# Kernel optimization log

Hardware: AMD Instinct MI355X
Metric: run time of the kernel (lower is better)

## Reference

```python
import jax, jax.numpy as jnp
import numpy as np

B, S, IN_DIM, D, H, L = 2, 2048, 64, 512, 8, 2
DK = D // H
EPS = 1e-5

def _layernorm(x, g, b):
    mu = jnp.mean(x, axis=-1, keepdims=True)
    var = jnp.mean((x - mu) ** 2, axis=-1, keepdims=True)
    return (x - mu) * jax.lax.rsqrt(var + EPS) * g + b

def _prob_sparse_layer(x, Wq, bq, Wk, bk, Wv, bv, fcW, fcb, ln_g, ln_b):
    # x: [B, S, D]
    Bs, Ss, _ = x.shape
    Q = (x @ Wq + bq).reshape(Bs, Ss, H, DK).transpose(0, 2, 1, 3)  # [B,H,S,DK]
    K = (x @ Wk + bk).reshape(Bs, Ss, H, DK).transpose(0, 2, 1, 3)
    V = (x @ Wv + bv).reshape(Bs, Ss, H, DK).transpose(0, 2, 1, 3)
    scores = jnp.einsum('bhqd,bhkd->bhqk', Q, K) / np.sqrt(DK).astype(np.float32)
    k = max(1, Ss // 10)
    top_scores, _ = jax.lax.top_k(scores, k)          # [B,H,S,k]
    threshold = top_scores[..., -1:]                  # k-th largest per row
    sparse_scores = jnp.where(scores < threshold, -jnp.inf, scores)
    attn = jax.nn.softmax(sparse_scores, axis=-1)     # dropout is identity in eval
    out = jnp.einsum('bhqk,bhkd->bhqd', attn, V)
    out = out.transpose(0, 2, 1, 3).reshape(Bs, Ss, D)
    out = out @ fcW + fcb
    return _layernorm(x + out, ln_g, ln_b)

def setup_inputs() -> dict:
    key = jax.random.key(0)
    ks = jax.random.split(key, 16)
    sd = 1.0 / np.sqrt(D)
    sdi = 1.0 / np.sqrt(IN_DIM)
    return {
        'x': jax.random.normal(ks[0], (B, S, IN_DIM), jnp.float32),
        'enc_W': jax.random.normal(ks[1], (IN_DIM, D), jnp.float32) * sdi,
        'enc_b': jnp.zeros((D,), jnp.float32),
        'Wq': jax.random.normal(ks[2], (L, D, D), jnp.float32) * sd,
        'bq': jnp.zeros((L, D), jnp.float32),
        'Wk': jax.random.normal(ks[3], (L, D, D), jnp.float32) * sd,
        'bk': jnp.zeros((L, D), jnp.float32),
        'Wv': jax.random.normal(ks[4], (L, D, D), jnp.float32) * sd,
        'bv': jnp.zeros((L, D), jnp.float32),
        'fcW': jax.random.normal(ks[5], (L, D, D), jnp.float32) * sd,
        'fcb': jnp.zeros((L, D), jnp.float32),
        'ln_g': jnp.ones((L, D), jnp.float32),
        'ln_b': jnp.zeros((L, D), jnp.float32),
        'dec_W': jax.random.normal(ks[6], (D, IN_DIM), jnp.float32) * sd,
        'dec_b': jnp.zeros((IN_DIM,), jnp.float32),
    }

def reference(x, enc_W, enc_b, Wq, bq, Wk, bk, Wv, bv, fcW, fcb, ln_g, ln_b, dec_W, dec_b):
    h = x @ enc_W + enc_b  # [B,S,D]
    for i in range(Wq.shape[0]):
        h = _prob_sparse_layer(h, Wq[i], bq[i], Wk[i], bk[i], Wv[i], bv[i],
                               fcW[i], fcb[i], ln_g[i], ln_b[i])
    return h[:, -1, :] @ dec_W + dec_b  # [B, IN_DIM]
```

## Files before the change

### kernel.cpp

```cpp
#include <hip/hip_runtime.h>
#include <hip/hip_bf16.h>

typedef unsigned short u16;
typedef __bf16 bf16x8 __attribute__((ext_vector_type(8)));
typedef u16 u16x8 __attribute__((ext_vector_type(8)));
typedef float f32x4 __attribute__((ext_vector_type(4)));

#define S_LEN 2048
#define NH 8
#define DMODEL 512
#define TOPK 204

__device__ __forceinline__ u16 f2b(float f) {
  __hip_bfloat16 h = __float2bfloat16(f);
  return __builtin_bit_cast(u16, h);
}
__device__ __forceinline__ unsigned f2b_fast(float f) {
  unsigned u = __float_as_uint(f);
  return (u + 0x7FFFu + ((u >> 16) & 1u)) >> 16;
}
__device__ __forceinline__ float kunmap(unsigned k) {
  unsigned tb = (k & 0x8000u) ? (k ^ 0x8000u) : (~k & 0xFFFFu);
  return __uint_as_float(tb << 16);
}
__device__ __forceinline__ unsigned fkmap(float f) {
  unsigned b = __float_as_uint(f) >> 16;
  return b ^ ((b & 0x8000u) ? 0xFFFFu : 0x8000u);
}

__global__ void transpose_w(const float* __restrict__ in, u16* __restrict__ out, int R, int C) {
  __shared__ float tile[32][33];
  int c0 = blockIdx.x * 32, r0 = blockIdx.y * 32;
  int tx = threadIdx.x & 31, ty = threadIdx.x >> 5;
#pragma unroll
  for (int i = 0; i < 32; i += 8)
    tile[ty + i][tx] = in[(long long)(r0 + ty + i) * C + c0 + tx];
  __syncthreads();
#pragma unroll
  for (int i = 0; i < 32; i += 8)
    out[(long long)(c0 + ty + i) * R + r0 + tx] = f2b(tile[tx][ty + i]);
}

__global__ void transpose_w4(const float* __restrict__ W0, const float* __restrict__ W1,
                             const float* __restrict__ W2, const float* __restrict__ W3,
                             u16* __restrict__ O0, u16* __restrict__ O1,
                             u16* __restrict__ O2, u16* __restrict__ O3) {
  __shared__ float tile[32][33];
  const float* in;
  u16* out;
  switch (blockIdx.z) {
    case 0: in = W0; out = O0; break;
    case 1: in = W1; out = O1; break;
    case 2: in = W2; out = O2; break;
    default: in = W3; out = O3; break;
  }
  int c0 = blockIdx.x * 32, r0 = blockIdx.y * 32;
  int tx = threadIdx.x & 31, ty = threadIdx.x >> 5;
#pragma unroll
  for (int i = 0; i < 32; i += 8)
    tile[ty + i][tx] = in[(long long)(r0 + ty + i) * 512 + c0 + tx];
  __syncthreads();
#pragma unroll
  for (int i = 0; i < 32; i += 8)
    out[(long long)(c0 + ty + i) * 512 + r0 + tx] = f2b(tile[tx][ty + i]);
}

__global__ void conv_b(const float* __restrict__ in, u16* __restrict__ out, int n) {
  int i = blockIdx.x * 256 + threadIdx.x;
  if (i < n) out[i] = f2b(in[i]);
}

template <int MODE>
__global__ __launch_bounds__(256) void gemm_bt(
    const u16* __restrict__ A, const u16* __restrict__ BT,
    const float* __restrict__ bias, const float* __restrict__ biasK, const float* __restrict__ biasV,
    float* __restrict__ outF, u16* __restrict__ outB, u16* __restrict__ outBK, u16* __restrict__ outBV,
    int M, int N, int K, float scale) {
  __shared__ u16 As[64 * 32];
  __shared__ u16 Bs[128 * 32];
  int n0 = blockIdx.x * 128, m0 = blockIdx.y * 64;
  int t = threadIdx.x;
  int lane = t & 63, wv = t >> 6;
  int mw = (wv & 1) * 32, nw = (wv >> 1) * 64;
  int fr = lane & 15, fg = lane >> 4;
  f32x4 acc[2][4] = {};
  for (int kt = 0; kt < K; kt += 32) {
    int e0 = t * 8;
    int r0r = e0 >> 5, c0c = e0 & 31;
    int e1 = e0 + 2048;
    int r1r = e1 >> 5, c1c = e1 & 31;
    *(u16x8*)&As[e0] = *(const u16x8*)&A[(long long)(m0 + r0r) * K + kt + c0c];
    *(u16x8*)&Bs[e0] = *(const u16x8*)&BT[(long long)(n0 + r0r) * K + kt + c0c];
    *(u16x8*)&Bs[e1] = *(const u16x8*)&BT[(long long)(n0 + r1r) * K + kt + c1c];
    __syncthreads();
    bf16x8 af[2], bfv[4];
#pragma unroll
    for (int i = 0; i < 2; i++) af[i] = *(const bf16x8*)&As[(mw + i * 16 + fr) * 32 + fg * 8];
#pragma unroll
    for (int j = 0; j < 4; j++) bfv[j] = *(const bf16x8*)&Bs[(nw + j * 16 + fr) * 32 + fg * 8];
#pragma unroll
    for (int i = 0; i < 2; i++)
#pragma unroll
      for (int j = 0; j < 4; j++)
        acc[i][j] = __builtin_amdgcn_mfma_f32_16x16x32_bf16(af[i], bfv[j], acc[i][j], 0, 0, 0);
    __syncthreads();
  }
#pragma unroll
  for (int i = 0; i < 2; i++)
#pragma unroll
    for (int j = 0; j < 4; j++) {
      int mloc = mw + i * 16 + fg * 4;
      int n = n0 + nw + j * 16 + fr;
      float bvl;
      if constexpr (MODE == 5) {
        int seg = n >> 9, nn = n & 511;
        bvl = (seg == 0 ? bias : seg == 1 ? biasK : biasV)[nn];
      } else {
        bvl = bias ? bias[n] : 0.f;
      }
#pragma unroll
      for (int r = 0; r < 4; r++) {
        int m = m0 + mloc + r;
        float v = acc[i][j][r] * scale + bvl;
        if constexpr (MODE == 0) {
          outF[(long long)m * N + n] = v;
        } else if constexpr (MODE == 4) {
          outF[(long long)m * N + n] = v;
          outB[(long long)m * N + n] = f2b(v);
        } else if constexpr (MODE == 5) {
          int seg = n >> 9, nn = n & 511;
          if (seg == 0) v *= 0.125f;
          u16 val = f2b(v);
          if (seg == 2) {
            outBV[((long long)((m >> 11) * NH + (nn >> 6)) * 64 + (nn & 63)) * S_LEN + (m & 2047)] = val;
          } else {
            long long qkidx = (long long)((m >> 11) * NH + (nn >> 6)) * (S_LEN * 64) +
                              (long long)(m & 2047) * 64 + (nn & 63);
            if (seg == 0) outB[qkidx] = val;
            else outBK[qkidx] = val;
          }
        }
      }
    }
}

__global__ __launch_bounds__(1024, 8) void score_pv(
    const u16* __restrict__ Qb, const u16* __restrict__ Kb, const u16* __restrict__ VTb,
    u16* __restrict__ aoB) {
  __shared__ u16 Qs[16 * 64];
  __shared__ __align__(16) u16 Ss[16 * 2048];
  __shared__ float thrS[16];
  __shared__ float mS[16];
  __shared__ float zS[16 * 16];
  int flat = blockIdx.x;
  int xcd = flat & 7, local = flat >> 3;
  int bh = xcd * 2 + (local >> 7);
  int m0 = (local & 127) * 16;
  int t = threadIdx.x;
  int lane = t & 63, wv = t >> 6, fr = lane & 15, fg = lane >> 4;
  const u16* Qg = Qb + ((long long)bh * S_LEN + m0) * 64;
  const u16* Kg = Kb + (long long)bh * S_LEN * 64;
  const u16* Vg = VTb + (long long)bh * 64 * S_LEN;
  if (t < 128) {
    int row = t >> 3, cc = t & 7;
    *(u16x8*)&Qs[row * 64 + ((cc ^ (row & 7)) * 8)] = *(const u16x8*)&Qg[row * 64 + cc * 8];
  }
  __syncthreads();
  bf16x8 aq[2];
#pragma unroll
  for (int ks = 0; ks < 2; ks++)
    aq[ks] = *(const bf16x8*)&Qs[fr * 64 + (((fg + 4 * ks) ^ (fr & 7)) * 8)];

#pragma unroll 4
  for (int tt = 0; tt < 8; tt++) {
    int col0 = wv * 128 + tt * 16;
    f32x4 acc = {};
#pragma unroll
    for (int ks = 0; ks < 2; ks++) {
      bf16x8 bk = *(const bf16x8*)&Kg[(long long)(col0 + fr) * 64 + ks * 32 + fg * 8];
      acc = __builtin_amdgcn_mfma_f32_16x16x32_bf16(bk, aq[ks], acc, 0, 0, 0);
    }
    uint2 w;
    w.x = f2b_fast(acc[0]) | (f2b_fast(acc[1]) << 16);
    w.y = f2b_fast(acc[2]) | (f2b_fast(acc[3]) << 16);
    int row = fr, col = col0 + fg * 4;
    *(uint2*)&Ss[row * 2048 + (col ^ ((row & 15) << 3))] = w;
  }
  __syncthreads();

  {
    int rr = wv;
    const uint2* cu2 = (const uint2*)&Ss[rr * 2048];
    float kf[32];
#pragma unroll
    for (int j = 0; j < 8; j++) {
      uint2 w = cu2[lane + 64 * j];
      kf[4 * j + 0] = __uint_as_float(w.x << 16);
      kf[4 * j + 1] = __uint_as_float(w.x & 0xFFFF0000u);
      kf[4 * j + 2] = __uint_as_float(w.y << 16);
      kf[4 * j + 3] = __uint_as_float(w.y & 0xFFFF0000u);
    }
    float mxf = kf[0];
#pragma unroll
    for (int j = 1; j < 32; j++) mxf = fmaxf(mxf, kf[j]);
#pragma unroll
    for (int o = 1; o < 64; o <<= 1)
      mxf = fmaxf(mxf, __uint_as_float((unsigned)__shfl_xor((int)__float_as_uint(mxf), o)));
    unsigned mxi = fkmap(mxf);
    unsigned lo, hi;
    unsigned lo0 = mxi > 384u ? mxi - 384u : 0u;
    {
      float pf = kunmap(lo0);
      int c = 0;
#pragma unroll
      for (int j = 0; j < 32; j++) c += (int)__popcll(__ballot(kf[j] >= pf));
      if (c >= TOPK) { lo = lo0; hi = mxi; }
      else { lo = 0u; hi = lo0 - 1u; }
    }
    while (lo < hi) {
      unsigned mid = (lo + hi + 1u) >> 1;
      float midf = kunmap(mid);
      int c = 0;
#pragma unroll
      for (int j = 0; j < 32; j++) c += (int)__popcll(__ballot(kf[j] >= midf));
      if (c >= TOPK) lo = mid; else hi = mid - 1u;
    }
    if (lane == 0) {
      thrS[rr] = kunmap(lo);
      mS[rr] = mxf;
    }
  }
  __syncthreads();

  float thrF = thrS[fr];
  float myM = mS[fr];
  float zpart = 0.f;
  f32x4 acc_o[4] = {};
#pragma unroll 2
  for (int step = 0; step < 4; step++) {
    int k0 = wv * 128 + step * 32;
    u16x8 kk = *(const u16x8*)&Ss[fr * 2048 + ((k0 + fg * 8) ^ ((fr & 15) << 3))];
    unsigned wp[4];
#pragma unroll
    for (int e2 = 0; e2 < 4; e2++) {
      float s0 = __uint_as_float((unsigned)kk[2 * e2] << 16);
      float s1 = __uint_as_float((unsigned)kk[2 * e2 + 1] << 16);
      float p0 = (s0 >= thrF) ? __expf(s0 - myM) : 0.f;
      float p1 = (s1 >= thrF) ? __expf(s1 - myM) : 0.f;
      zpart += p0 + p1;
      wp[e2] = f2b_fast(p0) | (f2b_fast(p1) << 16);
    }
    bf16x8 pa = *(bf16x8*)&wp;
#pragma unroll
    for (int j = 0; j < 4; j++) {
      bf16x8 bv = *(const bf16x8*)&Vg[(long long)(j * 16 + fr) * 2048 + k0 + fg * 8];
      acc_o[j] = __builtin_amdgcn_mfma_f32_16x16x32_bf16(pa, bv, acc_o[j], 0, 0, 0);
    }
  }
  zpart += __shfl_xor(zpart, 16);
  zpart += __shfl_xor(zpart, 32);
  __syncthreads();

  float* Of = (float*)Ss;
#pragma unroll
  for (int j = 0; j < 4; j++)
#pragma unroll
    for (int r = 0; r < 4; r++) {
      int row = fg * 4 + r, col = j * 16 + fr;
      Of[wv * 1024 + row * 64 + (col ^ ((row >> 2) << 3))] = acc_o[j][r];
    }
  if (fg == 0) zS[wv * 16 + fr] = zpart;
  __syncthreads();
  long long ob = (long long)(bh >> 3) * S_LEN * DMODEL + (bh & 7) * 64;
  {
    int row = t >> 6, dk = t & 63;
    int sw = dk ^ ((row >> 2) << 3);
    float s = 0.f;
#pragma unroll
    for (int w = 0; w < 16; w++) s += Of[w * 1024 + row * 64 + sw];
    float z = 0.f;
#pragma unroll
    for (int w = 0; w < 16; w++) z += zS[w * 16 + row];
    aoB[ob + (long long)(m0 + row) * DMODEL + dk] = f2b(s / z);
  }
}

__global__ __launch_bounds__(256) void resid_ln(const float* __restrict__ h, const float* __restrict__ fco,
                                                const float* __restrict__ g, const float* __restrict__ b,
                                                float* __restrict__ hout, u16* __restrict__ hbout) {
  __shared__ float red[4];
  int row = blockIdx.x;
  int t = threadIdx.x;
  long long base = (long long)row * 512;
  float v0 = h[base + t] + fco[base + t];
  float v1 = h[base + t + 256] + fco[base + t + 256];
  float s = v0 + v1;
#pragma unroll
  for (int o = 32; o > 0; o >>= 1) s += __shfl_down(s, o);
  if ((t & 63) == 0) red[t >> 6] = s;
  __syncthreads();
  float mu = (red[0] + red[1] + red[2] + red[3]) * (1.f / 512.f);
  float d0 = v0 - mu, d1 = v1 - mu;
  float q = d0 * d0 + d1 * d1;
#pragma unroll
  for (int o = 32; o > 0; o >>= 1) q += __shfl_down(q, o);
  __syncthreads();
  if ((t & 63) == 0) red[t >> 6] = q;
  __syncthreads();
  float var = (red[0] + red[1] + red[2] + red[3]) * (1.f / 512.f);
  float rs = rsqrtf(var + 1e-5f);
  float y0 = d0 * rs * g[t] + b[t];
  float y1 = d1 * rs * g[t + 256] + b[t + 256];
  hout[base + t] = y0;
  hout[base + t + 256] = y1;
  hbout[base + t] = f2b(y0);
  hbout[base + t + 256] = f2b(y1);
}

__global__ void decoder_k(const float* __restrict__ h, const float* __restrict__ W,
                          const float* __restrict__ bias, float* __restrict__ out) {
  int t = threadIdx.x;
  int b = t >> 6, j = t & 63;
  const float* hr = h + ((long long)b * S_LEN + (S_LEN - 1)) * DMODEL;
  float s = 0.f;
  for (int d = 0; d < DMODEL; d++) s += hr[d] * W[(long long)d * 64 + j];
  out[t] = s + bias[j];
}

extern "C" void kernel_launch(void* const* d_in, const int* in_sizes, int n_in,
                              void* d_out, int out_size, void* d_ws, size_t ws_size,
                              hipStream_t stream) {
  const float* x = (const float*)d_in[0];
  const float* enc_W = (const float*)d_in[1];
  const float* enc_b = (const float*)d_in[2];
  const float* Wq = (const float*)d_in[3];
  const float* bq = (const float*)d_in[4];
  const float* Wk = (const float*)d_in[5];
  const float* bk = (const float*)d_in[6];
  const float* Wv = (const float*)d_in[7];
  const float* bv = (const float*)d_in[8];
  const float* fcW = (const float*)d_in[9];
  const float* fcb = (const float*)d_in[10];
  const float* ln_g = (const float*)d_in[11];
  const float* ln_b = (const float*)d_in[12];
  const float* dec_W = (const float*)d_in[13];
  const float* dec_b = (const float*)d_in[14];

  char* p = (char*)d_ws;
  auto alloc = [&](size_t bytes) {
    char* r = p;
    p += (bytes + 255) & ~(size_t)255;
    return r;
  };
  const size_t BS = 2 * (size_t)S_LEN;
  u16* encWT = (u16*)alloc(512 * 64 * 2);
  u16* xbf = (u16*)alloc(BS * 64 * 2);
  float* hF = (float*)alloc(BS * 512 * 4);
  u16* hB = (u16*)alloc(BS * 512 * 2);
  u16* WqT = (u16*)alloc(512 * 512 * 2);
  u16* WkT = (u16*)alloc(512 * 512 * 2);
  u16* WvT = (u16*)alloc(512 * 512 * 2);
  u16* fcWT = (u16*)alloc(512 * 512 * 2);
  u16* Qb = (u16*)alloc((size_t)16 * 2048 * 64 * 2);
  u16* Kb = (u16*)alloc((size_t)16 * 2048 * 64 * 2);
  u16* VTb = (u16*)alloc((size_t)16 * 2048 * 64 * 2);
  u16* aoB = (u16*)alloc(BS * 512 * 2);
  float* fcO = (float*)Qb;

  transpose_w<<<dim3(16, 2), 256, 0, stream>>>(enc_W, encWT, 64, 512);
  conv_b<<<(int)(BS * 64 / 256), 256, 0, stream>>>(x, xbf, (int)(BS * 64));
  gemm_bt<4><<<dim3(4, 64), 256, 0, stream>>>(xbf, encWT, enc_b, nullptr, nullptr,
                                              hF, hB, nullptr, nullptr, 4096, 512, 64, 1.f);

  for (int l = 0; l < 2; l++) {
    transpose_w4<<<dim3(16, 16, 4), 256, 0, stream>>>(
        Wq + (size_t)l * 512 * 512, Wk + (size_t)l * 512 * 512,
        Wv + (size_t)l * 512 * 512, fcW + (size_t)l * 512 * 512,
        WqT, WkT, WvT, fcWT);
    gemm_bt<5><<<dim3(12, 64), 256, 0, stream>>>(hB, WqT, bq + l * 512, bk + l * 512, bv + l * 512,
                                                 nullptr, Qb, Kb, VTb, 4096, 1536, 512, 1.f);
    score_pv<<<dim3(2048), 1024, 0, stream>>>(Qb, Kb, VTb, aoB);
    gemm_bt<0><<<dim3(4, 64), 256, 0, stream>>>(aoB, fcWT, fcb + l * 512, nullptr, nullptr,
                                                fcO, nullptr, nullptr, nullptr, 4096, 512, 512, 1.f);
    resid_ln<<<4096, 256, 0, stream>>>(hF, fcO, ln_g + l * 512, ln_b + l * 512, hF, hB);
  }
  decoder_k<<<1, 128, 0, stream>>>(hF, dec_W, dec_b, (float*)d_out);
}
```

Measured before the change: 391.9 us.

## Use direct global-to-LDS loads in GEMM, MFMA priority hints, and a parallel decoder

The GEMM tile loads now use global_load_lds, which moves data straight into LDS instead of staging it through registers. In the score/PV kernel, the K and V fragment loads are hoisted ahead of the MFMA groups, and those groups are wrapped in s_setprio to raise wave priority during matrix math. The decoder is split across 2 blocks of 512 threads, with a shared-memory reduction over the D dimension replacing a serial loop of 512 steps. The top-k search initialization also gets a small cleanup. The goal is less register traffic and latency, at the risk of LDS-load ordering or sync subtleties.

```diff
diff --git a/kernel.cpp b/kernel.cpp
--- a/kernel.cpp
+++ b/kernel.cpp
@@ -26,6 +26,11 @@
 __device__ __forceinline__ unsigned fkmap(float f) {
   unsigned b = __float_as_uint(f) >> 16;
   return b ^ ((b & 0x8000u) ? 0xFFFFu : 0x8000u);
+}
+__device__ __forceinline__ void gload_lds16(const u16* g, u16* l) {
+  __builtin_amdgcn_global_load_lds(
+      (const __attribute__((address_space(1))) unsigned int*)(unsigned long long)(uintptr_t)g,
+      (__attribute__((address_space(3))) unsigned int*)(unsigned)(uintptr_t)l, 16, 0, 0);
 }
 
 __global__ void transpose_w(const float* __restrict__ in, u16* __restrict__ out, int R, int C) {
@@ -83,15 +88,15 @@
   int lane = t & 63, wv = t >> 6;
   int mw = (wv & 1) * 32, nw = (wv >> 1) * 64;
   int fr = lane & 15, fg = lane >> 4;
+  int e0 = t * 8;
+  int r0r = e0 >> 5, c0c = e0 & 31;
+  int e1 = e0 + 2048;
+  int r1r = e1 >> 5, c1c = e1 & 31;
   f32x4 acc[2][4] = {};
   for (int kt = 0; kt < K; kt += 32) {
-    int e0 = t * 8;
-    int r0r = e0 >> 5, c0c = e0 & 31;
-    int e1 = e0 + 2048;
-    int r1r = e1 >> 5, c1c = e1 & 31;
-    *(u16x8*)&As[e0] = *(const u16x8*)&A[(long long)(m0 + r0r) * K + kt + c0c];
-    *(u16x8*)&Bs[e0] = *(const u16x8*)&BT[(long long)(n0 + r0r) * K + kt + c0c];
-    *(u16x8*)&Bs[e1] = *(const u16x8*)&BT[(long long)(n0 + r1r) * K + kt + c1c];
+    gload_lds16(&A[(long long)(m0 + r0r) * K + kt + c0c], &As[e0]);
+    gload_lds16(&BT[(long long)(n0 + r0r) * K + kt + c0c], &Bs[e0]);
+    gload_lds16(&BT[(long long)(n0 + r1r) * K + kt + c1c], &Bs[e1]);
     __syncthreads();
     bf16x8 af[2], bfv[4];
 #pragma unroll
@@ -175,16 +180,17 @@
   for (int tt = 0; tt < 8; tt++) {
     int col0 = wv * 128 + tt * 16;
     f32x4 acc = {};
-#pragma unroll
-    for (int ks = 0; ks < 2; ks++) {
-      bf16x8 bk = *(const bf16x8*)&Kg[(long long)(col0 + fr) * 64 + ks * 32 + fg * 8];
-      acc = __builtin_amdgcn_mfma_f32_16x16x32_bf16(bk, aq[ks], acc, 0, 0, 0);
-    }
+    bf16x8 bk0 = *(const bf16x8*)&Kg[(long long)(col0 + fr) * 64 + fg * 8];
+    bf16x8 bk1 = *(const bf16x8*)&Kg[(long long)(col0 + fr) * 64 + 32 + fg * 8];
+    __builtin_amdgcn_s_setprio(1);
+    acc = __builtin_amdgcn_mfma_f32_16x16x32_bf16(bk0, aq[0], acc, 0, 0, 0);
+    acc = __builtin_amdgcn_mfma_f32_16x16x32_bf16(bk1, aq[1], acc, 0, 0, 0);
+    __builtin_amdgcn_s_setprio(0);
     uint2 w;
     w.x = f2b_fast(acc[0]) | (f2b_fast(acc[1]) << 16);
     w.y = f2b_fast(acc[2]) | (f2b_fast(acc[3]) << 16);
-    int row = fr, col = col0 + fg * 4;
-    *(uint2*)&Ss[row * 2048 + (col ^ ((row & 15) << 3))] = w;
+    int col = col0 + fg * 4;
+    *(uint2*)&Ss[fr * 2048 + (col ^ ((fr & 15) << 3))] = w;
   }
   __syncthreads();
 
@@ -208,14 +214,16 @@
       mxf = fmaxf(mxf, __uint_as_float((unsigned)__shfl_xor((int)__float_as_uint(mxf), o)));
     unsigned mxi = fkmap(mxf);
     unsigned lo, hi;
-    unsigned lo0 = mxi > 384u ? mxi - 384u : 0u;
-    {
+    if (mxi > 384u) {
+      unsigned lo0 = mxi - 384u;
       float pf = kunmap(lo0);
       int c = 0;
 #pragma unroll
       for (int j = 0; j < 32; j++) c += (int)__popcll(__ballot(kf[j] >= pf));
       if (c >= TOPK) { lo = lo0; hi = mxi; }
       else { lo = 0u; hi = lo0 - 1u; }
+    } else {
+      lo = 0u; hi = mxi;
     }
     while (lo < hi) {
       unsigned mid = (lo + hi + 1u) >> 1;
@@ -251,11 +259,16 @@
       wp[e2] = f2b_fast(p0) | (f2b_fast(p1) << 16);
     }
     bf16x8 pa = *(bf16x8*)&wp;
-#pragma unroll
-    for (int j = 0; j < 4; j++) {
-      bf16x8 bv = *(const bf16x8*)&Vg[(long long)(j * 16 + fr) * 2048 + k0 + fg * 8];
-      acc_o[j] = __builtin_amdgcn_mfma_f32_16x16x32_bf16(pa, bv, acc_o[j], 0, 0, 0);
-    }
+    bf16x8 bv0 = *(const bf16x8*)&Vg[(long long)(0 * 16 + fr) * 2048 + k0 + fg * 8];
+    bf16x8 bv1 = *(const bf16x8*)&Vg[(long long)(1 * 16 + fr) * 2048 + k0 + fg * 8];
+    bf16x8 bv2 = *(const bf16x8*)&Vg[(long long)(2 * 16 + fr) * 2048 + k0 + fg * 8];
+    bf16x8 bv3 = *(const bf16x8*)&Vg[(long long)(3 * 16 + fr) * 2048 + k0 + fg * 8];
+    __builtin_amdgcn_s_setprio(1);
+    acc_o[0] = __builtin_amdgcn_mfma_f32_16x16x32_bf16(pa, bv0, acc_o[0], 0, 0, 0);
+    acc_o[1] = __builtin_amdgcn_mfma_f32_16x16x32_bf16(pa, bv1, acc_o[1], 0, 0, 0);
+    acc_o[2] = __builtin_amdgcn_mfma_f32_16x16x32_bf16(pa, bv2, acc_o[2], 0, 0, 0);
+    acc_o[3] = __builtin_amdgcn_mfma_f32_16x16x32_bf16(pa, bv3, acc_o[3], 0, 0, 0);
+    __builtin_amdgcn_s_setprio(0);
   }
   zpart += __shfl_xor(zpart, 16);
   zpart += __shfl_xor(zpart, 32);
@@ -317,14 +330,24 @@
   hbout[base + t + 256] = f2b(y1);
 }
 
-__global__ void decoder_k(const float* __restrict__ h, const float* __restrict__ W,
-                          const float* __restrict__ bias, float* __restrict__ out) {
+__global__ __launch_bounds__(512) void decoder_k(const float* __restrict__ h, const float* __restrict__ W,
+                                                 const float* __restrict__ bias, float* __restrict__ out) {
+  __shared__ float part[8][64];
+  int b = blockIdx.x;
   int t = threadIdx.x;
-  int b = t >> 6, j = t & 63;
+  int j = t & 63, ds = t >> 6;
   const float* hr = h + ((long long)b * S_LEN + (S_LEN - 1)) * DMODEL;
   float s = 0.f;
-  for (int d = 0; d < DMODEL; d++) s += hr[d] * W[(long long)d * 64 + j];
-  out[t] = s + bias[j];
+#pragma unroll 8
+  for (int d = ds * 64; d < ds * 64 + 64; d++) s += hr[d] * W[(long long)d * 64 + j];
+  part[ds][j] = s;
+  __syncthreads();
+  if (t < 64) {
+    float acc = part[0][t];
+#pragma unroll
+    for (int w = 1; w < 8; w++) acc += part[w][t];
+    out[b * 64 + t] = acc + bias[t];
+  }
 }
 
 extern "C" void kernel_launch(void* const* d_in, const int* in_sizes, int n_in,
@@ -384,5 +407,5 @@
                                                 fcO, nullptr, nullptr, nullptr, 4096, 512, 512, 1.f);
     resid_ln<<<4096, 256, 0, stream>>>(hF, fcO, ln_g + l * 512, ln_b + l * 512, hF, hB);
   }
-  decoder_k<<<1, 128, 0, stream>>>(hF, dec_W, dec_b, (float*)d_out);
-}
+  decoder_k<<<2, 512, 0, stream>>>(hF, dec_W, dec_b, (float*)d_out);
+}
```

Result: faster. 368.6 us (-5.9%).
